# Performance work log

Measured on AMD Instinct MI355X. Metric: run time of the kernel, lower is better.

Reference implementation:

```python
import jax, jax.numpy as jnp
import numpy as np

N, E = 50000, 800000
IN_DIM, HID, HEADS, OUT_DIM = 128, 64, 4, 40
NEG_SLOPE = 0.2


def setup_inputs() -> dict:
    key = jax.random.key(0)
    ks = jax.random.split(key, 12)
    x = jax.random.normal(ks[0], (N, IN_DIM), dtype=jnp.float32)
    edge_index = jax.random.randint(ks[1], (2, E), 0, N, dtype=jnp.int64)
    timesteps = jax.random.randint(ks[2], (N,), 0, 100, dtype=jnp.int64)
    s = 1.0 / np.sqrt(IN_DIM)
    W_proj = jax.random.uniform(ks[3], (IN_DIM, HID), jnp.float32, -s, s)
    b_proj = jnp.zeros((HID,), jnp.float32)
    time_emb = jax.random.normal(ks[4], (100, HID), dtype=jnp.float32)
    sg = 1.0 / np.sqrt(HID)
    W_gat = jax.random.uniform(ks[5], (HID, HEADS * HID), jnp.float32, -sg, sg)
    att_src = jax.random.uniform(ks[6], (HEADS, HID), jnp.float32, -sg, sg)
    att_dst = jax.random.uniform(ks[7], (HEADS, HID), jnp.float32, -sg, sg)
    b_gat = jnp.zeros((HEADS * HID,), jnp.float32)
    sc = 1.0 / np.sqrt(HEADS * HID)
    W_cls = jax.random.uniform(ks[8], (HEADS * HID, OUT_DIM), jnp.float32, -sc, sc)
    b_cls = jnp.zeros((OUT_DIM,), jnp.float32)
    return {"x": x, "edge_index": edge_index, "timesteps": timesteps,
            "W_proj": W_proj, "b_proj": b_proj, "time_emb": time_emb,
            "W_gat": W_gat, "att_src": att_src, "att_dst": att_dst, "b_gat": b_gat,
            "W_cls": W_cls, "b_cls": b_cls}


def reference(x, edge_index, timesteps, W_proj, b_proj, time_emb,
              W_gat, att_src, att_dst, b_gat, W_cls, b_cls):
    n = x.shape[0]
    # feature projection + ReLU + time embedding
    h0 = jax.nn.relu(x @ W_proj + b_proj) + time_emb[timesteps]  # [N, HID]
    # --- GATConv (PyG semantics, add_self_loops=True, concat heads) ---
    h = (h0 @ W_gat).reshape(n, HEADS, HID)              # [N, H, C]
    a_src = jnp.einsum('nhc,hc->nh', h, att_src)         # [N, H]
    a_dst = jnp.einsum('nhc,hc->nh', h, att_dst)
    loops = jnp.arange(n, dtype=edge_index.dtype)
    src = jnp.concatenate([edge_index[0], loops])        # [E+N]
    dst = jnp.concatenate([edge_index[1], loops])
    e = jax.nn.leaky_relu(a_src[src] + a_dst[dst], NEG_SLOPE)  # [E+N, H]
    # segment softmax over incoming edges per destination node
    m = jax.ops.segment_max(e, dst, num_segments=n)      # [N, H]
    p = jnp.exp(e - m[dst])
    denom = jax.ops.segment_sum(p, dst, num_segments=n)  # [N, H]
    alpha = p / (denom[dst] + 1e-16)                     # [E+N, H]
    msg = alpha[:, :, None] * h[src]                     # [E+N, H, C]
    agg = jax.ops.segment_sum(msg, dst, num_segments=n)  # [N, H, C]
    gat_out = agg.reshape(n, HEADS * HID) + b_gat
    # ReLU + (dropout is identity in eval) + classifier
    return jax.nn.relu(gat_out) @ W_cls + b_cls          # [N, OUT_DIM]
```

## Files before the change

### kernel.cpp

```cpp
#include <hip/hip_runtime.h>
#include <hip/hip_fp16.h>

#define IN_DIM 128
#define HID 64
#define HEADS 4
#define OUT_DIM 40
#define CAP 64
#define NEG 0.2f
#define PA_EPB 4096
#define BKT_SH 9
#define BKT_CAP 10240
#define GPAD 264

__device__ __forceinline__ float lrelu(float v) { return v > 0.f ? v : NEG * v; }

union HU { float2 f2; __half2 h2[2]; };
union HU2 { float4 f4; __half2 h2[4]; };

typedef _Float16 h2v __attribute__((ext_vector_type(2)));
union DU { float4 f4; h2v h[4]; };

__device__ __forceinline__ float4 unpack_h4(float2 bits) {
    HU u; u.f2 = bits;
    float2 lo = __half22float2(u.h2[0]);
    float2 hi = __half22float2(u.h2[1]);
    return make_float4(lo.x, lo.y, hi.x, hi.y);
}

__global__ __launch_bounds__(256) void partA_kernel(
    const int* __restrict__ ei, int E, int nbkt, int paBlocks,
    int* __restrict__ cnt, unsigned int* __restrict__ ebuf,
    const float* __restrict__ Wg, const float* __restrict__ attS,
    const float* __restrict__ attD, const float* __restrict__ Wc,
    float* __restrict__ aSf, float* __restrict__ aDf,
    __half2* __restrict__ Wgp, __half* __restrict__ WcTg)
{
    if (blockIdx.x >= paBlocks) {
        int gid = (blockIdx.x - paBlocks) * 256 + threadIdx.x;
        if (gid < 256) {
            int k = gid >> 2, hd = gid & 3;
            const float* wr = Wg + k * 256 + hd * 64;
            const float* as = attS + hd * 64;
            const float* ad = attD + hd * 64;
            float ss = 0.f, dd = 0.f;
            for (int c = 0; c < 64; ++c) { float w = wr[c]; ss += w * as[c]; dd += w * ad[c]; }
            aSf[k * 4 + hd] = ss;
            aDf[k * 4 + hd] = dd;
        } else if (gid < 256 + 32 * 256) {
            int i = gid - 256;
            int kp = i >> 8, o = i & 255;
            Wgp[i] = __floats2half2_rn(Wg[(2 * kp) * 256 + o], Wg[(2 * kp + 1) * 256 + o]);
        } else if (gid < 256 + 32 * 256 + OUT_DIM * 256) {
            int i = gid - 256 - 32 * 256;
            int o = i >> 8, k = i & 255;
            WcTg[i] = __float2half(Wc[k * OUT_DIM + o]);
        }
        return;
    }

    __shared__ int localCnt[128];
    __shared__ int baseArr[128];
    for (int i = threadIdx.x; i < nbkt; i += 256) localCnt[i] = 0;
    __syncthreads();

    const int e0 = blockIdx.x * PA_EPB + threadIdx.x;
    unsigned short l[16];
#pragma unroll
    for (int j = 0; j < 16; ++j) {
        int e = e0 + j * 256;
        if (e < E) {
            int d = ei[E + e];
            l[j] = (unsigned short)atomicAdd(&localCnt[d >> BKT_SH], 1);
        }
    }
    __syncthreads();
    for (int i = threadIdx.x; i < nbkt; i += 256)
        baseArr[i] = atomicAdd(&cnt[i], localCnt[i]);
    __syncthreads();
#pragma unroll
    for (int j = 0; j < 16; ++j) {
        int e = e0 + j * 256;
        if (e < E) {
            int s = ei[e];
            int d = ei[E + e];
            int b = d >> BKT_SH;
            int off = baseArr[b] + (int)l[j];
            if (off < BKT_CAP)
                ebuf[(size_t)b * BKT_CAP + off] =
                    ((unsigned)(d & ((1 << BKT_SH) - 1)) << 16) | (unsigned)s;
        }
    }
}

__global__ __launch_bounds__(256) void partB_kernel(
    const unsigned int* __restrict__ ebuf, const int* __restrict__ cnt,
    int* __restrict__ deg, unsigned short* __restrict__ csr, int N)
{
    __shared__ int cntL[512];
    __shared__ unsigned short rows[512 * CAP];
    const int b = blockIdx.x;
    for (int i = threadIdx.x; i < 512; i += 256) cntL[i] = 0;
    __syncthreads();

    int cb = cnt[b]; cb = cb < BKT_CAP ? cb : BKT_CAP;
    const unsigned int* eb = ebuf + (size_t)b * BKT_CAP;
    for (int i = threadIdx.x; i < cb; i += 256) {
        unsigned v = eb[i];
        int dloc = v >> 16;
        int slot = atomicAdd(&cntL[dloc], 1);
        if (slot < CAP) rows[dloc * CAP + slot] = (unsigned short)(v & 0xFFFFu);
    }
    __syncthreads();

    const int d0 = b << BKT_SH;
    for (int i = threadIdx.x; i < 512; i += 256) {
        int d = d0 + i;
        if (d < N) deg[d] = cntL[i];
    }
    int limRows = N - d0; limRows = limRows < 512 ? limRows : 512;
    if (limRows <= 0) return;
    const uint4* rsrc = (const uint4*)rows;
    uint4* rdst = (uint4*)(csr + (size_t)d0 * CAP);
    int nvec = (limRows * CAP) >> 3;
    for (int i = threadIdx.x; i < nvec; i += 256)
        rdst[i] = rsrc[i];
}

__global__ __launch_bounds__(256) void proj_kernel(
    const float* __restrict__ x, const float* __restrict__ Wp,
    const float* __restrict__ bp, const float* __restrict__ temb,
    const int* __restrict__ ts, const float* __restrict__ aSf,
    const float* __restrict__ aDf,
    __half* __restrict__ h0h, float* __restrict__ aS, float* __restrict__ aD, int N)
{
    __shared__ __half Wl[IN_DIM * HID];
    for (int i = threadIdx.x * 8; i < IN_DIM * HID; i += 256 * 8) {
        float4 wa = *(const float4*)(Wp + i);
        float4 wb = *(const float4*)(Wp + i + 4);
        HU2 u;
        u.h2[0] = __floats2half2_rn(wa.x, wa.y);
        u.h2[1] = __floats2half2_rn(wa.z, wa.w);
        u.h2[2] = __floats2half2_rn(wb.x, wb.y);
        u.h2[3] = __floats2half2_rn(wb.z, wb.w);
        *(float4*)(Wl + i) = u.f4;
    }
    __syncthreads();

    const int t = threadIdx.x;
    const int lane = t & 63, wq = t >> 6;
    const int cg = lane & 15, ng = lane >> 4;
    const int c0 = cg * 4;
    const int nodeBase = blockIdx.x * 32 + wq * 8 + ng * 2;

    float4 acc[2];
#pragma unroll
    for (int j = 0; j < 2; ++j) acc[j] = make_float4(0.f, 0.f, 0.f, 0.f);

    for (int k0 = 0; k0 < IN_DIM; k0 += 4) {
        float4 xv[2];
#pragma unroll
        for (int j = 0; j < 2; ++j) {
            int n = nodeBase + j; n = n < N ? n : N - 1;
            xv[j] = *(const float4*)(x + (size_t)n * IN_DIM + k0);
        }
        float4 wv[4];
#pragma unroll
        for (int kk = 0; kk < 4; ++kk)
            wv[kk] = unpack_h4(*(const float2*)(Wl + (k0 + kk) * HID + c0));
#pragma unroll
        for (int j = 0; j < 2; ++j) {
            const float* xs = (const float*)&xv[j];
#pragma unroll
            for (int kk = 0; kk < 4; ++kk) {
                acc[j].x += xs[kk] * wv[kk].x;
                acc[j].y += xs[kk] * wv[kk].y;
                acc[j].z += xs[kk] * wv[kk].z;
                acc[j].w += xs[kk] * wv[kk].w;
            }
        }
    }
    const float4 bb = *(const float4*)(bp + c0);
    float4 s0 = *(const float4*)(aSf + (c0 + 0) * 4);
    float4 s1 = *(const float4*)(aSf + (c0 + 1) * 4);
    float4 s2 = *(const float4*)(aSf + (c0 + 2) * 4);
    float4 s3 = *(const float4*)(aSf + (c0 + 3) * 4);
    float4 d0 = *(const float4*)(aDf + (c0 + 0) * 4);
    float4 d1 = *(const float4*)(aDf + (c0 + 1) * 4);
    float4 d2 = *(const float4*)(aDf + (c0 + 2) * 4);
    float4 d3 = *(const float4*)(aDf + (c0 + 3) * 4);
#pragma unroll
    for (int j = 0; j < 2; ++j) {
        int n = nodeBase + j;
        float4 r = make_float4(0.f, 0.f, 0.f, 0.f);
        if (n < N) {
            int tv = ts[n];
            float4 te = *(const float4*)(temb + (size_t)tv * HID + c0);
            r.x = fmaxf(acc[j].x + bb.x, 0.f) + te.x;
            r.y = fmaxf(acc[j].y + bb.y, 0.f) + te.y;
            r.z = fmaxf(acc[j].z + bb.z, 0.f) + te.z;
            r.w = fmaxf(acc[j].w + bb.w, 0.f) + te.w;
            HU u;
            u.h2[0] = __floats2half2_rn(r.x, r.y);
            u.h2[1] = __floats2half2_rn(r.z, r.w);
            *(float2*)(h0h + (size_t)n * HID + c0) = u.f2;
        }
        float4 pS, pD;
        pS.x = r.x * s0.x + r.y * s1.x + r.z * s2.x + r.w * s3.x;
        pS.y = r.x * s0.y + r.y * s1.y + r.z * s2.y + r.w * s3.y;
        pS.z = r.x * s0.z + r.y * s1.z + r.z * s2.z + r.w * s3.z;
        pS.w = r.x * s0.w + r.y * s1.w + r.z * s2.w + r.w * s3.w;
        pD.x = r.x * d0.x + r.y * d1.x + r.z * d2.x + r.w * d3.x;
        pD.y = r.x * d0.y + r.y * d1.y + r.z * d2.y + r.w * d3.y;
        pD.z = r.x * d0.z + r.y * d1.z + r.z * d2.z + r.w * d3.z;
        pD.w = r.x * d0.w + r.y * d1.w + r.z * d2.w + r.w * d3.w;
#pragma unroll
        for (int off = 8; off > 0; off >>= 1) {
            pS.x += __shfl_down(pS.x, off); pS.y += __shfl_down(pS.y, off);
            pS.z += __shfl_down(pS.z, off); pS.w += __shfl_down(pS.w, off);
            pD.x += __shfl_down(pD.x, off); pD.y += __shfl_down(pD.y, off);
            pD.z += __shfl_down(pD.z, off); pD.w += __shfl_down(pD.w, off);
        }
        if (cg == 0 && n < N) {
            *(float4*)(aS + (size_t)n * 4) = pS;
            *(float4*)(aD + (size_t)n * 4) = pD;
        }
    }
}

__global__ __launch_bounds__(256) void agg_kernel(
    const __half* __restrict__ h0h, const float* __restrict__ aS,
    const float* __restrict__ aD, const int* __restrict__ deg,
    const unsigned short* __restrict__ csr, __half* __restrict__ agg0h, int N)
{
    __shared__ float p_lds[4 * CAP * HEADS];
    __shared__ int   s_lds[4 * CAP];

    const int t = threadIdx.x;
    const int lane = t & 63, wq = t >> 6;
    const int n = blockIdx.x * 4 + wq;
    if (n >= N) return;
    const int hd16 = lane >> 4, li = lane & 15;

    const float adn = aD[n * 4 + hd16];
    const float es = lrelu(aS[n * 4 + hd16] + adn);

    int dn = deg[n]; dn = dn < CAP ? dn : CAP;
    const unsigned short* cs = csr + (size_t)n * CAP;
    float* pL = p_lds + wq * CAP * HEADS;
    int*   sL = s_lds + wq * CAP;

    float m = -1e30f;
    for (int i = li; i < dn; i += 16) {
        int src = cs[i];
        if (hd16 == 0) sL[i] = src << 7;
        float e = lrelu(aS[src * 4 + hd16] + adn);
        pL[i * HEADS + hd16] = e;
        m = fmaxf(m, e);
    }
#pragma unroll
    for (int off = 8; off > 0; off >>= 1)
        m = fmaxf(m, __shfl_xor(m, off));
    m = fmaxf(m, es);
    float mh[4], esh[4];
#pragma unroll
    for (int h = 0; h < 4; ++h) {
        mh[h]  = __shfl(m, h * 16);
        esh[h] = __shfl(es, h * 16);
    }

    float sp = 0.f;
    for (int idx = lane; idx < dn * 4; idx += 64) {
        float p = __expf(pL[idx] - mh[idx & 3]);
        pL[idx] = p;
        sp += p;
    }
#pragma unroll
    for (int off = 4; off < 64; off <<= 1)
        sp += __shfl_xor(sp, off);
    float pselfh[4], invh[4];
#pragma unroll
    for (int h = 0; h < 4; ++h) {
        float sh = __shfl(sp, h);
        pselfh[h] = __expf(esh[h] - mh[h]);
        invh[h] = 1.f / (sh + pselfh[h] + 1e-16f);
    }

    const int half = lane >> 5;
    const int ch2 = lane & 31;
    const char* hb = (const char*)h0h;
    const int laneByte = ch2 << 2;

    float2 acc[4];
    {
        HU sv; sv.f2.x = 0.f;
        float lo = 0.f, hi = 0.f;
        if (half == 0) {
            __half2 v2 = *(const __half2*)(hb + ((size_t)n << 7) + laneByte);
            float2 f = __half22float2(v2);
            lo = f.x; hi = f.y;
        }
#pragma unroll
        for (int h = 0; h < 4; ++h) {
            acc[h].x = pselfh[h] * lo;
            acc[h].y = pselfh[h] * hi;
        }
        (void)sv;
    }
    int i = 0;
    for (; i + 8 <= dn; i += 8) {
        int off0 = sL[i + 0 + half];
        int off1 = sL[i + 2 + half];
        int off2 = sL[i + 4 + half];
        int off3 = sL[i + 6 + half];
        __half2 v0 = *(const __half2*)(hb + off0 + laneByte);
        __half2 v1 = *(const __half2*)(hb + off1 + laneByte);
        __half2 v2 = *(const __half2*)(hb + off2 + laneByte);
        __half2 v3 = *(const __half2*)(hb + off3 + laneByte);
        float4 p0 = *(const float4*)(pL + (i + 0 + half) * 4);
        float4 p1 = *(const float4*)(pL + (i + 2 + half) * 4);
        float4 p2 = *(const float4*)(pL + (i + 4 + half) * 4);
        float4 p3 = *(const float4*)(pL + (i + 6 + half) * 4);
        float2 f;
        f = __half22float2(v0);
        acc[0].x += p0.x * f.x; acc[0].y += p0.x * f.y;
        acc[1].x += p0.y * f.x; acc[1].y += p0.y * f.y;
        acc[2].x += p0.z * f.x; acc[2].y += p0.z * f.y;
        acc[3].x += p0.w * f.x; acc[3].y += p0.w * f.y;
        f = __half22float2(v1);
        acc[0].x += p1.x * f.x; acc[0].y += p1.x * f.y;
        acc[1].x += p1.y * f.x; acc[1].y += p1.y * f.y;
        acc[2].x += p1.z * f.x; acc[2].y += p1.z * f.y;
        acc[3].x += p1.w * f.x; acc[3].y += p1.w * f.y;
        f = __half22float2(v2);
        acc[0].x += p2.x * f.x; acc[0].y += p2.x * f.y;
        acc[1].x += p2.y * f.x; acc[1].y += p2.y * f.y;
        acc[2].x += p2.z * f.x; acc[2].y += p2.z * f.y;
        acc[3].x += p2.w * f.x; acc[3].y += p2.w * f.y;
        f = __half22float2(v3);
        acc[0].x += p3.x * f.x; acc[0].y += p3.x * f.y;
        acc[1].x += p3.y * f.x; acc[1].y += p3.y * f.y;
        acc[2].x += p3.z * f.x; acc[2].y += p3.z * f.y;
        acc[3].x += p3.w * f.x; acc[3].y += p3.w * f.y;
    }
    for (; i + 2 <= dn; i += 2) {
        int off0 = sL[i + half];
        __half2 v0 = *(const __half2*)(hb + off0 + laneByte);
        float4 p0 = *(const float4*)(pL + (i + half) * 4);
        float2 f = __half22float2(v0);
        acc[0].x += p0.x * f.x; acc[0].y += p0.x * f.y;
        acc[1].x += p0.y * f.x; acc[1].y += p0.y * f.y;
        acc[2].x += p0.z * f.x; acc[2].y += p0.z * f.y;
        acc[3].x += p0.w * f.x; acc[3].y += p0.w * f.y;
    }
    if (i < dn && half == 0) {
        int off0 = sL[i];
        __half2 v0 = *(const __half2*)(hb + off0 + laneByte);
        float4 p0 = *(const float4*)(pL + i * 4);
        float2 f = __half22float2(v0);
        acc[0].x += p0.x * f.x; acc[0].y += p0.x * f.y;
        acc[1].x += p0.y * f.x; acc[1].y += p0.y * f.y;
        acc[2].x += p0.z * f.x; acc[2].y += p0.z * f.y;
        acc[3].x += p0.w * f.x; acc[3].y += p0.w * f.y;
    }
#pragma unroll
    for (int h = 0; h < 4; ++h) {
        acc[h].x += __shfl_xor(acc[h].x, 32);
        acc[h].y += __shfl_xor(acc[h].y, 32);
    }
    if (lane < 32) {
        __half2* dst = (__half2*)(agg0h + (size_t)n * 256);
#pragma unroll
        for (int h = 0; h < 4; ++h)
            dst[h * 32 + ch2] = __floats2half2_rn(acc[h].x * invh[h],
                                                  acc[h].y * invh[h]);
    }
}

__global__ __launch_bounds__(256) void gatcls_kernel(
    const __half* __restrict__ agg0h, const __half2* __restrict__ Wgp,
    const float* __restrict__ bg, const __half* __restrict__ WcTg,
    const float* __restrict__ bc, float* __restrict__ out, int N)
{
    __shared__ __half WcT[OUT_DIM * GPAD];
    __shared__ __half gtile[32 * GPAD];

    for (int i = threadIdx.x * 8; i < OUT_DIM * 256; i += 256 * 8)
        *(float4*)(WcT + (i >> 8) * GPAD + (i & 255)) = *(const float4*)(WcTg + i);
    __syncthreads();

    const int t = threadIdx.x;
    const int lane = t & 63, wq = t >> 6;
    const int c0 = lane * 4;
    const int headBase = (c0 >> 6) << 6;
    const int nodeBase = blockIdx.x * 32 + wq * 8;

    float4 acc[8];
#pragma unroll
    for (int j = 0; j < 8; ++j) acc[j] = make_float4(0.f, 0.f, 0.f, 0.f);

    for (int k0 = 0; k0 < HID; k0 += 8) {
        const int kp0 = k0 >> 1;
        DU wv[4];
#pragma unroll
        for (int p = 0; p < 4; ++p)
            wv[p].f4 = *(const float4*)(Wgp + (kp0 + p) * 256 + c0);
#pragma unroll
        for (int j = 0; j < 8; ++j) {
            int n = nodeBase + j; n = n < N ? n : N - 1;
            DU xr; xr.f4 = *(const float4*)(agg0h + (size_t)n * 256 + headBase + k0);
#pragma unroll
            for (int p = 0; p < 4; ++p) {
                acc[j].x = __builtin_amdgcn_fdot2(xr.h[p], wv[p].h[0], acc[j].x, false);
                acc[j].y = __builtin_amdgcn_fdot2(xr.h[p], wv[p].h[1], acc[j].y, false);
                acc[j].z = __builtin_amdgcn_fdot2(xr.h[p], wv[p].h[2], acc[j].z, false);
                acc[j].w = __builtin_amdgcn_fdot2(xr.h[p], wv[p].h[3], acc[j].w, false);
            }
        }
    }
    const float4 b4 = *(const float4*)(bg + c0);
#pragma unroll
    for (int j = 0; j < 8; ++j) {
        int jn = wq * 8 + j;
        HU u;
        u.h2[0] = __floats2half2_rn(fmaxf(acc[j].x + b4.x, 0.f),
                                    fmaxf(acc[j].y + b4.y, 0.f));
        u.h2[1] = __floats2half2_rn(fmaxf(acc[j].z + b4.z, 0.f),
                                    fmaxf(acc[j].w + b4.w, 0.f));
        *(float2*)(gtile + jn * GPAD + c0) = u.f2;
    }
    __syncthreads();

    const int nodeLoc = t >> 3;
    const int og = t & 7;
    const int n = blockIdx.x * 32 + nodeLoc;
    float acc5[5] = {0.f, 0.f, 0.f, 0.f, 0.f};
    for (int kb = 0; kb < 256; kb += 8) {
        DU gb; gb.f4 = *(const float4*)(gtile + nodeLoc * GPAD + kb);
#pragma unroll
        for (int i = 0; i < 5; ++i) {
            DU wb; wb.f4 = *(const float4*)(WcT + (og * 5 + i) * GPAD + kb);
#pragma unroll
            for (int p = 0; p < 4; ++p)
                acc5[i] = __builtin_amdgcn_fdot2(gb.h[p], wb.h[p], acc5[i], false);
        }
    }
    if (n < N) {
#pragma unroll
        for (int i = 0; i < 5; ++i) {
            int o = og * 5 + i;
            out[(size_t)n * OUT_DIM + o] = acc5[i] + bc[o];
        }
    }
}

extern "C" void kernel_launch(void* const* d_in, const int* in_sizes, int n_in,
                              void* d_out, int out_size, void* d_ws, size_t ws_size,
                              hipStream_t stream) {
    const float* x    = (const float*)d_in[0];
    const int*   ei   = (const int*)d_in[1];
    const int*   ts   = (const int*)d_in[2];
    const float* Wp   = (const float*)d_in[3];
    const float* bp   = (const float*)d_in[4];
    const float* temb = (const float*)d_in[5];
    const float* Wg   = (const float*)d_in[6];
    const float* attS = (const float*)d_in[7];
    const float* attD = (const float*)d_in[8];
    const float* bg   = (const float*)d_in[9];
    const float* Wc   = (const float*)d_in[10];
    const float* bc   = (const float*)d_in[11];
    float* out = (float*)d_out;

    const int N = in_sizes[0] / IN_DIM;
    const int E = in_sizes[1] / 2;
    const int nbkt = (N + (1 << BKT_SH) - 1) >> BKT_SH;

    char* w = (char*)d_ws;
    __half*         h0h   = (__half*)w;         w += (size_t)N * HID * 2;
    __half*         agg0h = (__half*)w;         w += (size_t)N * 256 * 2;
    float*          aS    = (float*)w;          w += (size_t)N * HEADS * 4;
    float*          aD    = (float*)w;          w += (size_t)N * HEADS * 4;
    int*            deg   = (int*)w;            w += (size_t)N * 4;
    unsigned short* csr   = (unsigned short*)w; w += (size_t)N * CAP * 2;
    unsigned int*   ebuf  = (unsigned int*)w;   w += (size_t)nbkt * BKT_CAP * 4;
    int*            cnt   = (int*)w;            w += (size_t)nbkt * 4;
    float*          aSf   = (float*)w;          w += 256 * 4;
    float*          aDf   = (float*)w;          w += 256 * 4;
    __half2*        Wgp   = (__half2*)w;        w += (size_t)32 * 256 * 4;
    __half*         WcTg  = (__half*)w;         w += (size_t)OUT_DIM * 256 * 2;

    const int paBlocks = (E + PA_EPB - 1) / PA_EPB;
    const int prepWork = 256 + 32 * 256 + OUT_DIM * 256;
    const int prepBlocks = (prepWork + 255) / 256;

    hipMemsetAsync(cnt, 0, (size_t)nbkt * 4, stream);
    partA_kernel<<<paBlocks + prepBlocks, 256, 0, stream>>>(
        ei, E, nbkt, paBlocks, cnt, ebuf, Wg, attS, attD, Wc, aSf, aDf, Wgp, WcTg);
    partB_kernel<<<nbkt, 256, 0, stream>>>(ebuf, cnt, deg, csr, N);
    proj_kernel<<<(N + 31) / 32, 256, 0, stream>>>(x, Wp, bp, temb, ts, aSf, aDf,
                                                   h0h, aS, aD, N);
    agg_kernel<<<(N + 3) / 4, 256, 0, stream>>>(h0h, aS, aD, deg, csr, agg0h, N);
    gatcls_kernel<<<(N + 31) / 32, 256, 0, stream>>>(agg0h, Wgp, bg, WcTg, bc, out, N);
}
```

Baseline: 217.1 us.

## Use MFMA f16 matrix instructions for GAT linear and classifier in gatcls kernel

```diff
diff --git a/kernel.cpp b/kernel.cpp
--- a/kernel.cpp
+++ b/kernel.cpp
@@ -20,6 +20,10 @@
 typedef _Float16 h2v __attribute__((ext_vector_type(2)));
 union DU { float4 f4; h2v h[4]; };
 
+typedef _Float16 f16x8 __attribute__((ext_vector_type(8)));
+typedef float f32x4 __attribute__((ext_vector_type(4)));
+union FU { float4 f4; f16x8 v; };
+
 __device__ __forceinline__ float4 unpack_h4(float2 bits) {
     HU u; u.f2 = bits;
     float2 lo = __half22float2(u.h2[0]);
@@ -33,7 +37,7 @@
     const float* __restrict__ Wg, const float* __restrict__ attS,
     const float* __restrict__ attD, const float* __restrict__ Wc,
     float* __restrict__ aSf, float* __restrict__ aDf,
-    __half2* __restrict__ Wgp, __half* __restrict__ WcTg)
+    __half* __restrict__ WgT, __half* __restrict__ WcTg)
 {
     if (blockIdx.x >= paBlocks) {
         int gid = (blockIdx.x - paBlocks) * 256 + threadIdx.x;
@@ -46,12 +50,12 @@
             for (int c = 0; c < 64; ++c) { float w = wr[c]; ss += w * as[c]; dd += w * ad[c]; }
             aSf[k * 4 + hd] = ss;
             aDf[k * 4 + hd] = dd;
-        } else if (gid < 256 + 32 * 256) {
+        } else if (gid < 256 + 256 * HID) {
             int i = gid - 256;
-            int kp = i >> 8, o = i & 255;
-            Wgp[i] = __floats2half2_rn(Wg[(2 * kp) * 256 + o], Wg[(2 * kp + 1) * 256 + o]);
-        } else if (gid < 256 + 32 * 256 + OUT_DIM * 256) {
-            int i = gid - 256 - 32 * 256;
+            int o = i >> 6, k = i & 63;
+            WgT[i] = __float2half(Wg[k * 256 + o]);
+        } else if (gid < 256 + 256 * HID + OUT_DIM * 256) {
+            int i = gid - 256 - 256 * HID;
             int o = i >> 8, k = i & 255;
             WcTg[i] = __float2half(Wc[k * OUT_DIM + o]);
         }
@@ -292,7 +296,6 @@
 
     float2 acc[4];
     {
-        HU sv; sv.f2.x = 0.f;
         float lo = 0.f, hi = 0.f;
         if (half == 0) {
             __half2 v2 = *(const __half2*)(hb + ((size_t)n << 7) + laneByte);
@@ -304,7 +307,6 @@
             acc[h].x = pselfh[h] * lo;
             acc[h].y = pselfh[h] * hi;
         }
-        (void)sv;
     }
     int i = 0;
     for (; i + 8 <= dn; i += 8) {
@@ -377,78 +379,89 @@
 }
 
 __global__ __launch_bounds__(256) void gatcls_kernel(
-    const __half* __restrict__ agg0h, const __half2* __restrict__ Wgp,
+    const __half* __restrict__ agg0h, const __half* __restrict__ WgT,
     const float* __restrict__ bg, const __half* __restrict__ WcTg,
     const float* __restrict__ bc, float* __restrict__ out, int N)
 {
-    __shared__ __half WcT[OUT_DIM * GPAD];
     __shared__ __half gtile[32 * GPAD];
-
-    for (int i = threadIdx.x * 8; i < OUT_DIM * 256; i += 256 * 8)
-        *(float4*)(WcT + (i >> 8) * GPAD + (i & 255)) = *(const float4*)(WcTg + i);
-    __syncthreads();
 
     const int t = threadIdx.x;
     const int lane = t & 63, wq = t >> 6;
-    const int c0 = lane * 4;
-    const int headBase = (c0 >> 6) << 6;
-    const int nodeBase = blockIdx.x * 32 + wq * 8;
-
-    float4 acc[8];
-#pragma unroll
-    for (int j = 0; j < 8; ++j) acc[j] = make_float4(0.f, 0.f, 0.f, 0.f);
-
-    for (int k0 = 0; k0 < HID; k0 += 8) {
-        const int kp0 = k0 >> 1;
-        DU wv[4];
-#pragma unroll
-        for (int p = 0; p < 4; ++p)
-            wv[p].f4 = *(const float4*)(Wgp + (kp0 + p) * 256 + c0);
-#pragma unroll
-        for (int j = 0; j < 8; ++j) {
-            int n = nodeBase + j; n = n < N ? n : N - 1;
-            DU xr; xr.f4 = *(const float4*)(agg0h + (size_t)n * 256 + headBase + k0);
-#pragma unroll
-            for (int p = 0; p < 4; ++p) {
-                acc[j].x = __builtin_amdgcn_fdot2(xr.h[p], wv[p].h[0], acc[j].x, false);
-                acc[j].y = __builtin_amdgcn_fdot2(xr.h[p], wv[p].h[1], acc[j].y, false);
-                acc[j].z = __builtin_amdgcn_fdot2(xr.h[p], wv[p].h[2], acc[j].z, false);
-                acc[j].w = __builtin_amdgcn_fdot2(xr.h[p], wv[p].h[3], acc[j].w, false);
+    const int m16 = lane & 15, quad = lane >> 4;
+    const int nodeBase = blockIdx.x * 32;
+
+    {
+        const int h = wq;
+        f32x4 acc[2][4];
+#pragma unroll
+        for (int mt = 0; mt < 2; ++mt)
+#pragma unroll
+            for (int nt = 0; nt < 4; ++nt)
+                acc[mt][nt] = (f32x4){0.f, 0.f, 0.f, 0.f};
+
+#pragma unroll
+        for (int ks = 0; ks < 2; ++ks) {
+            FU a[2], b[4];
+#pragma unroll
+            for (int mt = 0; mt < 2; ++mt) {
+                int n = nodeBase + mt * 16 + m16; n = n < N ? n : N - 1;
+                a[mt].f4 = *(const float4*)(agg0h + (size_t)n * 256 + h * 64 + ks * 32 + quad * 8);
             }
-        }
-    }
-    const float4 b4 = *(const float4*)(bg + c0);
-#pragma unroll
-    for (int j = 0; j < 8; ++j) {
-        int jn = wq * 8 + j;
-        HU u;
-        u.h2[0] = __floats2half2_rn(fmaxf(acc[j].x + b4.x, 0.f),
-                                    fmaxf(acc[j].y + b4.y, 0.f));
-        u.h2[1] = __floats2half2_rn(fmaxf(acc[j].z + b4.z, 0.f),
-                                    fmaxf(acc[j].w + b4.w, 0.f));
-        *(float2*)(gtile + jn * GPAD + c0) = u.f2;
-    }
-    __syncthreads();
-
-    const int nodeLoc = t >> 3;
-    const int og = t & 7;
-    const int n = blockIdx.x * 32 + nodeLoc;
-    float acc5[5] = {0.f, 0.f, 0.f, 0.f, 0.f};
-    for (int kb = 0; kb < 256; kb += 8) {
-        DU gb; gb.f4 = *(const float4*)(gtile + nodeLoc * GPAD + kb);
-#pragma unroll
-        for (int i = 0; i < 5; ++i) {
-            DU wb; wb.f4 = *(const float4*)(WcT + (og * 5 + i) * GPAD + kb);
-#pragma unroll
-            for (int p = 0; p < 4; ++p)
-                acc5[i] = __builtin_amdgcn_fdot2(gb.h[p], wb.h[p], acc5[i], false);
-        }
-    }
-    if (n < N) {
-#pragma unroll
-        for (int i = 0; i < 5; ++i) {
-            int o = og * 5 + i;
-            out[(size_t)n * OUT_DIM + o] = acc5[i] + bc[o];
+#pragma unroll
+            for (int nt = 0; nt < 4; ++nt) {
+                int o = h * 64 + nt * 16 + m16;
+                b[nt].f4 = *(const float4*)(WgT + o * 64 + ks * 32 + quad * 8);
+            }
+#pragma unroll
+            for (int mt = 0; mt < 2; ++mt)
+#pragma unroll
+                for (int nt = 0; nt < 4; ++nt)
+                    acc[mt][nt] = __builtin_amdgcn_mfma_f32_16x16x32_f16(
+                        a[mt].v, b[nt].v, acc[mt][nt], 0, 0, 0);
+        }
+#pragma unroll
+        for (int nt = 0; nt < 4; ++nt) {
+            int o = h * 64 + nt * 16 + m16;
+            float bv = bg[o];
+#pragma unroll
+            for (int mt = 0; mt < 2; ++mt) {
+#pragma unroll
+                for (int r = 0; r < 4; ++r) {
+                    int nloc = mt * 16 + quad * 4 + r;
+                    gtile[nloc * GPAD + o] = __float2half(fmaxf(acc[mt][nt][r] + bv, 0.f));
+                }
+            }
+        }
+    }
+    __syncthreads();
+
+    {
+        const int mt = wq >> 1;
+        const int ntCount = (wq & 1) ? 1 : 2;
+        const int ntBase = (wq & 1) ? 2 : 0;
+        f32x4 acc2[2];
+        acc2[0] = (f32x4){0.f, 0.f, 0.f, 0.f};
+        acc2[1] = (f32x4){0.f, 0.f, 0.f, 0.f};
+#pragma unroll
+        for (int ks = 0; ks < 8; ++ks) {
+            FU a; a.f4 = *(const float4*)(gtile + (mt * 16 + m16) * GPAD + ks * 32 + quad * 8);
+            for (int q = 0; q < ntCount; ++q) {
+                int o = (ntBase + q) * 16 + m16;
+                int oc = o < OUT_DIM ? o : OUT_DIM - 1;
+                FU b; b.f4 = *(const float4*)(WcTg + oc * 256 + ks * 32 + quad * 8);
+                acc2[q] = __builtin_amdgcn_mfma_f32_16x16x32_f16(a.v, b.v, acc2[q], 0, 0, 0);
+            }
+        }
+        for (int q = 0; q < ntCount; ++q) {
+            int o = (ntBase + q) * 16 + m16;
+            if (o < OUT_DIM) {
+                float bv = bc[o];
+#pragma unroll
+                for (int r = 0; r < 4; ++r) {
+                    int n = nodeBase + mt * 16 + quad * 4 + r;
+                    if (n < N) out[(size_t)n * OUT_DIM + o] = acc2[q][r] + bv;
+                }
+            }
         }
     }
 }
@@ -485,19 +498,19 @@
     int*            cnt   = (int*)w;            w += (size_t)nbkt * 4;
     float*          aSf   = (float*)w;          w += 256 * 4;
     float*          aDf   = (float*)w;          w += 256 * 4;
-    __half2*        Wgp   = (__half2*)w;        w += (size_t)32 * 256 * 4;
+    __half*         WgT   = (__half*)w;         w += (size_t)256 * HID * 2;
     __half*         WcTg  = (__half*)w;         w += (size_t)OUT_DIM * 256 * 2;
 
     const int paBlocks = (E + PA_EPB - 1) / PA_EPB;
-    const int prepWork = 256 + 32 * 256 + OUT_DIM * 256;
+    const int prepWork = 256 + 256 * HID + OUT_DIM * 256;
     const int prepBlocks = (prepWork + 255) / 256;
 
     hipMemsetAsync(cnt, 0, (size_t)nbkt * 4, stream);
     partA_kernel<<<paBlocks + prepBlocks, 256, 0, stream>>>(
-        ei, E, nbkt, paBlocks, cnt, ebuf, Wg, attS, attD, Wc, aSf, aDf, Wgp, WcTg);
+        ei, E, nbkt, paBlocks, cnt, ebuf, Wg, attS, attD, Wc, aSf, aDf, WgT, WcTg);
     partB_kernel<<<nbkt, 256, 0, stream>>>(ebuf, cnt, deg, csr, N);
     proj_kernel<<<(N + 31) / 32, 256, 0, stream>>>(x, Wp, bp, temb, ts, aSf, aDf,
                                                    h0h, aS, aD, N);
     agg_kernel<<<(N + 3) / 4, 256, 0, stream>>>(h0h, aS, aD, deg, csr, agg0h, N);
-    gatcls_kernel<<<(N + 31) / 32, 256, 0, stream>>>(agg0h, Wgp, bg, WcTg, bc, out, N);
-}
+    gatcls_kernel<<<(N + 31) / 32, 256, 0, stream>>>(agg0h, WgT, bg, WcTg, bc, out, N);
+}
```

New measurement: 211.2 us. 2.7% less time.
